# Kernel tuning notes

Measured on AMD Instinct MI355X. Metric: run time of the kernel, lower is better.

## Reference

```python
import jax, jax.numpy as jnp
import numpy as np

# --- configuration constants (from OpticalDotProductConfiguration) ---
INPUT_BITS = 8
ADC_BITS = 8
DAC_VMIN, DAC_VMAX = 0.0, 1.0
ADC_VMAX = 1.0
OPT_GAIN = 10.0
AWG_XTALK = 0.01
MZM_VMIN, MZM_VMAX = 0.0, 1.0
MZM_LOSS = 10.0 ** (-0.5 / 10.0)   # loss_dB_to_linear(0.5)
YB_LOSS = 10.0 ** (-0.3 / 10.0)
MRR_LOSS = 10.0 ** (-0.5 / 10.0)
MRR_XTALK = 0.01
PD_RESP = 1.0
PD_DARK = 1e-12
PD_R = 50.0
PD_HZ = 10.0 * 1e9
PD_T = 300.0
TIA_GAIN = 100.0
K_B = 1.380649e-23
Q_E = 1.602176634e-19

B, N = 4096, 8192


def conv_same(x, kernel):
    # x: [B, N], kernel: [K]; torch F.conv1d = cross-correlation, same as lax conv
    out = jax.lax.conv_general_dilated(
        x[:, None, :], kernel[None, None, :], (1,), 'SAME')
    return out[:, 0, :]


def setup_inputs() -> dict:
    key = jax.random.key(0)
    ks = jax.random.split(key, 6)
    return {
        'x': jax.random.normal(ks[0], (B, N), dtype=jnp.float32),
        'weights': jax.random.normal(ks[1], (N,), dtype=jnp.float32),
        'noise_tp': jax.random.normal(ks[2], (B,), dtype=jnp.float32),
        'noise_sp': jax.random.normal(ks[3], (B,), dtype=jnp.float32),
        'noise_tn': jax.random.normal(ks[4], (B,), dtype=jnp.float32),
        'noise_sn': jax.random.normal(ks[5], (B,), dtype=jnp.float32),
    }


def reference(x, weights, noise_tp, noise_sp, noise_tn, noise_sn):
    dt = x.dtype
    # software_implemented_transformation
    wnorm = jnp.max(jnp.abs(weights))
    wnorm = jnp.where(wnorm <= 1e-9, jnp.asarray(1.0, dt), wnorm)
    wt = weights / wnorm
    w_abs = jnp.abs(wt)            # weight DAC is identity for weights
    w_pos = wt >= 0                # [N] bool

    t_pos = x > 0                  # [B, N]
    ax = jnp.abs(x)
    inorm = jnp.max(ax, axis=1)
    inorm = jnp.where(inorm <= 1e-9, jnp.asarray(1.0, dt), inorm)[:, None]
    maxq_in = 2 ** INPUT_BITS - 1
    q = jnp.round(ax / inorm * maxq_in)

    # input DAC
    d = jnp.round(jnp.clip(q, 0.0, maxq_in)) / maxq_in
    d = DAC_VMIN + (DAC_VMAX - DAC_VMIN) * d

    # laser: gain + AWG crosstalk conv
    lk = jnp.array([AWG_XTALK / 4, AWG_XTALK, 1.0, AWG_XTALK, AWG_XTALK / 4], dtype=dt)
    l = conv_same(d * OPT_GAIN, lk)

    # MZM
    m = l * w_abs / (MZM_VMAX - MZM_VMIN) * (YB_LOSS * MZM_LOSS)

    # MRR: masked split, crosstalk conv, loss, reduce over N
    pm = jnp.logical_not(jnp.logical_xor(w_pos[None, :], t_pos)).astype(dt)
    mk = jnp.array([MRR_XTALK / 4, MRR_XTALK, 1.0, MRR_XTALK, MRR_XTALK / 4], dtype=dt)
    pos_sum = jnp.sum(conv_same(m * pm, mk) * MRR_LOSS, axis=1)        # [B]
    neg_sum = jnp.sum(conv_same(m * (1.0 - pm), mk) * MRR_LOSS, axis=1)

    # photodiode with injected noise
    thermal_c = 4.0 * K_B * PD_T * PD_HZ / PD_R
    shot_c = 2.0 * Q_E * PD_HZ

    def pd(t, nth, nsh):
        t = t * PD_RESP + PD_DARK
        t = t + nth * thermal_c
        return t * (1.0 + nsh * shot_c)

    cur = pd(pos_sum, noise_tp, noise_sp) - pd(neg_sum, noise_tn, noise_sn)

    # TIA
    v = jnp.abs(cur * TIA_GAIN)
    sign = (cur >= 0).astype(dt) * 2.0 - 1.0

    # ADC
    sf = (2 ** ADC_BITS - 1) / ADC_VMAX
    va = jnp.round(jnp.clip(v, 0.0, ADC_VMAX) * sf) / sf
    out = va * sign

    scale = wnorm / (2.0 ** (ADC_BITS - INPUT_BITS))
    scale = scale / (OPT_GAIN * TIA_GAIN * MRR_LOSS * YB_LOSS * MZM_LOSS)
    scale = scale / ((PD_RESP + PD_RESP) / 2.0)
    out = out * (scale * inorm[:, 0])
    return out
```

## Files before the change

### kernel.cpp

```cpp
#include <hip/hip_runtime.h>
#include <math.h>

#define NCOL 8192
#define BT   512
#define EPT  16

#define MZM_LOSS_D 0.8912509381337456
#define YB_LOSS_D  0.9332543007969910
#define MRR_LOSS_D 0.8912509381337456

__global__ __launch_bounds__(BT, 4)
void odp_main(const float* __restrict__ x, const float* __restrict__ w,
              const float* __restrict__ ntp, const float* __restrict__ nsp,
              const float* __restrict__ ntn, const float* __restrict__ nsn,
              float* __restrict__ out)
{
    __shared__ float  redf[16];
    __shared__ float  redT[8];
    __shared__ double redD[8];
    __shared__ double corrd[4];

    const int t    = threadIdx.x;
    const int lane = t & 63;
    const int wid  = t >> 6;
    const int b    = blockIdx.x;

    const float v_ntp = ntp[b], v_nsp = nsp[b], v_ntn = ntn[b], v_nsn = nsn[b];

    const float*  __restrict__ xrow = x + (size_t)b * NCOL;
    const float4* __restrict__ xr4  = (const float4*)xrow;
    const float4* __restrict__ w4   = (const float4*)w;

    float xf[EPT], wf[EPT];
    const int hL = (t > 0)      ? (t * EPT - 2)   : 0;
    const int hR = (t < BT - 1) ? (t * EPT + EPT) : (NCOL - 2);
    const float2 hxL = *(const float2*)(xrow + hL);
    const float2 hxR = *(const float2*)(xrow + hR);

    float mx = 0.f, mw = 0.f;
#pragma unroll
    for (int j = 0; j < 4; ++j) {
        const float4 xv = xr4[t * 4 + j];
        const float4 wv = w4 [t * 4 + j];
        xf[4*j+0]=xv.x; xf[4*j+1]=xv.y; xf[4*j+2]=xv.z; xf[4*j+3]=xv.w;
        wf[4*j+0]=wv.x; wf[4*j+1]=wv.y; wf[4*j+2]=wv.z; wf[4*j+3]=wv.w;
        mx = fmaxf(mx, fmaxf(fmaxf(fabsf(xv.x), fabsf(xv.y)),
                             fmaxf(fabsf(xv.z), fabsf(xv.w))));
        mw = fmaxf(mw, fmaxf(fmaxf(fabsf(wv.x), fabsf(wv.y)),
                             fmaxf(fabsf(wv.z), fabsf(wv.w))));
    }
#pragma unroll
    for (int off = 32; off; off >>= 1) {
        mx = fmaxf(mx, __shfl_down(mx, off));
        mw = fmaxf(mw, __shfl_down(mw, off));
    }
    if (lane == 0) { redf[wid] = mx; redf[8 + wid] = mw; }
    __syncthreads();

    float inorm = redf[0], wnorm = redf[8];
#pragma unroll
    for (int i = 1; i < 8; ++i) {
        inorm = fmaxf(inorm, redf[i]);
        wnorm = fmaxf(wnorm, redf[8 + i]);
    }
    inorm = (inorm <= 1e-9f) ? 1.f : inorm;
    wnorm = (wnorm <= 1e-9f) ? 1.f : wnorm;

    const double inv_d = 1.0 / (double)inorm;
    const float  y     = (float)inv_d;

    float Q[EPT + 4];
#pragma unroll
    for (int c = 0; c < EPT; ++c) {
        const float a  = fabsf(xf[c]);
        const float q0 = a * y;
        const float r  = fmaf(-inorm, q0, a);
        Q[c + 2] = rintf(fmaf(r, y, q0) * 255.f);
    }
    {
        const float aL0 = fabsf(hxL.x), aL1 = fabsf(hxL.y);
        const float aR0 = fabsf(hxR.x), aR1 = fabsf(hxR.y);
        float q0, r;
        q0 = aL0 * y; r = fmaf(-inorm, q0, aL0); Q[0]  = rintf(fmaf(r, y, q0) * 255.f);
        q0 = aL1 * y; r = fmaf(-inorm, q0, aL1); Q[1]  = rintf(fmaf(r, y, q0) * 255.f);
        q0 = aR0 * y; r = fmaf(-inorm, q0, aR0); Q[18] = rintf(fmaf(r, y, q0) * 255.f);
        q0 = aR1 * y; r = fmaf(-inorm, q0, aR1); Q[19] = rintf(fmaf(r, y, q0) * 255.f);
        if (t == 0)      { Q[0]  = 0.f; Q[1]  = 0.f; }
        if (t == BT - 1) { Q[18] = 0.f; Q[19] = 0.f; }
    }

    float Dv[4] = {0.f,0.f,0.f,0.f}, Tv[4] = {0.f,0.f,0.f,0.f};
    double cD = 0.0, cT = 0.0;
    const double DE0 = -((double)0.01f + (double)0.0025f);
    const double DE1 = -((double)0.0025f);

#pragma unroll
    for (int c = 0; c < EPT; ++c) {
        const float s1 = Q[c + 1] + Q[c + 3];
        const float s2 = Q[c]     + Q[c + 4];
        float conv = fmaf(0.01f, s1, Q[c + 2]);
        conv = fmaf(0.0025f, s2, conv);
        const float sel = (xf[c] > 0.f) ? wf[c] : -wf[c];
        Dv[c & 3] = fmaf(conv, sel,        Dv[c & 3]);
        Tv[c & 3] = fmaf(conv, fabsf(sel), Tv[c & 3]);
        if (t == 0 && c < 2) {
            const double de = (c == 0) ? DE0 : DE1;
            cD += de * (double)(conv * sel);
            cT += de * (double)(conv * fabsf(sel));
        }
        if (t == BT - 1 && c >= EPT - 2) {
            const double de = (c == EPT - 1) ? DE0 : DE1;
            cD += de * (double)(conv * sel);
            cT += de * (double)(conv * fabsf(sel));
        }
    }

    double accD = ((double)Dv[0] + (double)Dv[1]) + ((double)Dv[2] + (double)Dv[3]);
    float  accT = (Tv[0] + Tv[1]) + (Tv[2] + Tv[3]);

#pragma unroll
    for (int off = 32; off; off >>= 1) {
        accD += __shfl_down(accD, off);
        accT += __shfl_down(accT, off);
    }
    if (lane == 0)   { redD[wid] = accD; redT[wid] = accT; }
    if (t == 0)      { corrd[0] = cD; corrd[1] = cT; }
    if (t == BT - 1) { corrd[2] = cD; corrd[3] = cT; }
    __syncthreads();

    if (t == 0) {
        double D = 0.0, T = 0.0;
#pragma unroll
        for (int i = 0; i < 8; ++i) { D += redD[i]; T += (double)redT[i]; }
        const double E_MID = 1.0 + 2.0 * (double)0.01f + 2.0 * (double)0.0025f;
        D = D * E_MID + (corrd[0] + corrd[2]);
        T = T * E_MID + (corrd[1] + corrd[3]);

        const double Kd = (10.0 / 255.0) * (YB_LOSS_D * MZM_LOSS_D) / (double)wnorm;
        const double ps = (T + D) * 0.5 * Kd * MRR_LOSS_D;
        const double ns = (T - D) * 0.5 * Kd * MRR_LOSS_D;

        const float thermal_f = 3.3135576e-12f;
        const float shot_f    = 3.204353268e-9f;

        double tp_ = ps + 1e-12 + (double)(v_ntp * thermal_f);
        tp_ *= (double)(1.0f + v_nsp * shot_f);
        double tn_ = ns + 1e-12 + (double)(v_ntn * thermal_f);
        tn_ *= (double)(1.0f + v_nsn * shot_f);

        const double cur = tp_ - tn_;
        double v = fabs(cur * 100.0);
        v = fmin(v, 1.0);
        const double va  = rint(v * 255.0) * (1.0 / 255.0);
        const double sgn = (cur >= 0.0) ? 1.0 : -1.0;
        const double scale = (double)wnorm /
            (10.0 * 100.0 * MRR_LOSS_D * YB_LOSS_D * MZM_LOSS_D);
        out[b] = (float)(va * sgn * scale * (double)inorm);
    }
}

extern "C" void kernel_launch(void* const* d_in, const int* in_sizes, int n_in,
                              void* d_out, int out_size, void* d_ws, size_t ws_size,
                              hipStream_t stream) {
    const float* x   = (const float*)d_in[0];
    const float* w   = (const float*)d_in[1];
    const float* ntp = (const float*)d_in[2];
    const float* nsp = (const float*)d_in[3];
    const float* ntn = (const float*)d_in[4];
    const float* nsn = (const float*)d_in[5];
    float* out = (float*)d_out;
    odp_main<<<dim3(out_size), dim3(BT), 0, stream>>>(x, w, ntp, nsp, ntn, nsn, out);
}
```

Baseline: 30.31 us.

## Halve block size, double elements per thread, defer weight-norm reduction

```diff
diff --git a/kernel.cpp b/kernel.cpp
--- a/kernel.cpp
+++ b/kernel.cpp
@@ -2,12 +2,24 @@
 #include <math.h>
 
 #define NCOL 8192
-#define BT   512
-#define EPT  16
+#define BT   256
+#define EPT  32
 
 #define MZM_LOSS_D 0.8912509381337456
 #define YB_LOSS_D  0.9332543007969910
 #define MRR_LOSS_D 0.8912509381337456
+
+static __device__ __forceinline__ void lds_barrier() {
+    asm volatile("s_waitcnt lgkmcnt(0)" ::: "memory");
+    __builtin_amdgcn_s_barrier();
+}
+
+#define QF(dst, a_) do {                                   \
+    const float a__  = (a_);                               \
+    const float q0__ = a__ * y;                            \
+    const float r__  = fmaf(-inorm, q0__, a__);            \
+    (dst) = rintf(fmaf(r__, y, q0__) * 255.f);             \
+} while (0)
 
 __global__ __launch_bounds__(BT, 4)
 void odp_main(const float* __restrict__ x, const float* __restrict__ w,
@@ -15,9 +27,10 @@
               const float* __restrict__ ntn, const float* __restrict__ nsn,
               float* __restrict__ out)
 {
-    __shared__ float  redf[16];
-    __shared__ float  redT[8];
-    __shared__ double redD[8];
+    __shared__ float  redX[4];
+    __shared__ float  redW[4];
+    __shared__ float  redT[4];
+    __shared__ double redD[4];
     __shared__ double corrd[4];
 
     const int t    = threadIdx.x;
@@ -32,88 +45,81 @@
     const float4* __restrict__ w4   = (const float4*)w;
 
     float xf[EPT], wf[EPT];
-    const int hL = (t > 0)      ? (t * EPT - 2)   : 0;
-    const int hR = (t < BT - 1) ? (t * EPT + EPT) : (NCOL - 2);
-    const float2 hxL = *(const float2*)(xrow + hL);
-    const float2 hxR = *(const float2*)(xrow + hR);
-
     float mx = 0.f, mw = 0.f;
 #pragma unroll
-    for (int j = 0; j < 4; ++j) {
-        const float4 xv = xr4[t * 4 + j];
-        const float4 wv = w4 [t * 4 + j];
+    for (int j = 0; j < 8; ++j) {
+        const float4 xv = xr4[t * 8 + j];
         xf[4*j+0]=xv.x; xf[4*j+1]=xv.y; xf[4*j+2]=xv.z; xf[4*j+3]=xv.w;
-        wf[4*j+0]=wv.x; wf[4*j+1]=wv.y; wf[4*j+2]=wv.z; wf[4*j+3]=wv.w;
         mx = fmaxf(mx, fmaxf(fmaxf(fabsf(xv.x), fabsf(xv.y)),
                              fmaxf(fabsf(xv.z), fabsf(xv.w))));
+    }
+    const float2 hxL = *(const float2*)(xrow + ((t > 0)      ? t*EPT - 2   : 0));
+    const float2 hxR = *(const float2*)(xrow + ((t < BT - 1) ? t*EPT + EPT : NCOL - 2));
+#pragma unroll
+    for (int j = 0; j < 8; ++j) {
+        const float4 wv = w4[t * 8 + j];
+        wf[4*j+0]=wv.x; wf[4*j+1]=wv.y; wf[4*j+2]=wv.z; wf[4*j+3]=wv.w;
         mw = fmaxf(mw, fmaxf(fmaxf(fabsf(wv.x), fabsf(wv.y)),
                              fmaxf(fabsf(wv.z), fabsf(wv.w))));
     }
+
 #pragma unroll
-    for (int off = 32; off; off >>= 1) {
+    for (int off = 32; off; off >>= 1)
         mx = fmaxf(mx, __shfl_down(mx, off));
-        mw = fmaxf(mw, __shfl_down(mw, off));
-    }
-    if (lane == 0) { redf[wid] = mx; redf[8 + wid] = mw; }
-    __syncthreads();
+    if (lane == 0) redX[wid] = mx;
+    lds_barrier();
 
-    float inorm = redf[0], wnorm = redf[8];
-#pragma unroll
-    for (int i = 1; i < 8; ++i) {
-        inorm = fmaxf(inorm, redf[i]);
-        wnorm = fmaxf(wnorm, redf[8 + i]);
-    }
+    float inorm = fmaxf(fmaxf(redX[0], redX[1]), fmaxf(redX[2], redX[3]));
     inorm = (inorm <= 1e-9f) ? 1.f : inorm;
-    wnorm = (wnorm <= 1e-9f) ? 1.f : wnorm;
-
     const double inv_d = 1.0 / (double)inorm;
     const float  y     = (float)inv_d;
-
-    float Q[EPT + 4];
-#pragma unroll
-    for (int c = 0; c < EPT; ++c) {
-        const float a  = fabsf(xf[c]);
-        const float q0 = a * y;
-        const float r  = fmaf(-inorm, q0, a);
-        Q[c + 2] = rintf(fmaf(r, y, q0) * 255.f);
-    }
-    {
-        const float aL0 = fabsf(hxL.x), aL1 = fabsf(hxL.y);
-        const float aR0 = fabsf(hxR.x), aR1 = fabsf(hxR.y);
-        float q0, r;
-        q0 = aL0 * y; r = fmaf(-inorm, q0, aL0); Q[0]  = rintf(fmaf(r, y, q0) * 255.f);
-        q0 = aL1 * y; r = fmaf(-inorm, q0, aL1); Q[1]  = rintf(fmaf(r, y, q0) * 255.f);
-        q0 = aR0 * y; r = fmaf(-inorm, q0, aR0); Q[18] = rintf(fmaf(r, y, q0) * 255.f);
-        q0 = aR1 * y; r = fmaf(-inorm, q0, aR1); Q[19] = rintf(fmaf(r, y, q0) * 255.f);
-        if (t == 0)      { Q[0]  = 0.f; Q[1]  = 0.f; }
-        if (t == BT - 1) { Q[18] = 0.f; Q[19] = 0.f; }
-    }
 
     float Dv[4] = {0.f,0.f,0.f,0.f}, Tv[4] = {0.f,0.f,0.f,0.f};
     double cD = 0.0, cT = 0.0;
     const double DE0 = -((double)0.01f + (double)0.0025f);
     const double DE1 = -((double)0.0025f);
 
-#pragma unroll
-    for (int c = 0; c < EPT; ++c) {
-        const float s1 = Q[c + 1] + Q[c + 3];
-        const float s2 = Q[c]     + Q[c + 4];
-        float conv = fmaf(0.01f, s1, Q[c + 2]);
-        conv = fmaf(0.0025f, s2, conv);
-        const float sel = (xf[c] > 0.f) ? wf[c] : -wf[c];
-        Dv[c & 3] = fmaf(conv, sel,        Dv[c & 3]);
-        Tv[c & 3] = fmaf(conv, fabsf(sel), Tv[c & 3]);
-        if (t == 0 && c < 2) {
-            const double de = (c == 0) ? DE0 : DE1;
-            cD += de * (double)(conv * sel);
-            cT += de * (double)(conv * fabsf(sel));
-        }
-        if (t == BT - 1 && c >= EPT - 2) {
-            const double de = (c == EPT - 1) ? DE0 : DE1;
-            cD += de * (double)(conv * sel);
-            cT += de * (double)(conv * fabsf(sel));
-        }
-    }
+#define HALF_BODY(H) do {                                                     \
+    float Q[20];                                                              \
+    if ((H) == 0) {                                                           \
+        QF(Q[0], fabsf(hxL.x)); QF(Q[1], fabsf(hxL.y));                       \
+        if (t == 0) { Q[0] = 0.f; Q[1] = 0.f; }                               \
+    } else {                                                                  \
+        QF(Q[0], fabsf(xf[14])); QF(Q[1], fabsf(xf[15]));                     \
+    }                                                                         \
+    _Pragma("unroll")                                                         \
+    for (int cc = 0; cc < 16; ++cc) QF(Q[cc + 2], fabsf(xf[(H)*16 + cc]));    \
+    if ((H) == 0) {                                                           \
+        QF(Q[18], fabsf(xf[16])); QF(Q[19], fabsf(xf[17]));                   \
+    } else {                                                                  \
+        QF(Q[18], fabsf(hxR.x)); QF(Q[19], fabsf(hxR.y));                     \
+        if (t == BT - 1) { Q[18] = 0.f; Q[19] = 0.f; }                        \
+    }                                                                         \
+    _Pragma("unroll")                                                         \
+    for (int cc = 0; cc < 16; ++cc) {                                         \
+        const int idx = (H)*16 + cc;                                          \
+        const float s1 = Q[cc + 1] + Q[cc + 3];                               \
+        const float s2 = Q[cc]     + Q[cc + 4];                               \
+        float cv = fmaf(0.01f, s1, Q[cc + 2]);                                \
+        cv = fmaf(0.0025f, s2, cv);                                           \
+        const float sel = (xf[idx] > 0.f) ? wf[idx] : -wf[idx];               \
+        Dv[cc & 3] = fmaf(cv, sel,        Dv[cc & 3]);                        \
+        Tv[cc & 3] = fmaf(cv, fabsf(sel), Tv[cc & 3]);                        \
+        if ((H) == 0 && t == 0 && cc < 2) {                                   \
+            const double de = (cc == 0) ? DE0 : DE1;                          \
+            cD += de * (double)(cv * sel);                                    \
+            cT += de * (double)(cv * fabsf(sel));                             \
+        }                                                                     \
+        if ((H) == 1 && t == BT - 1 && cc >= 14) {                            \
+            const double de = (cc == 15) ? DE0 : DE1;                         \
+            cD += de * (double)(cv * sel);                                    \
+            cT += de * (double)(cv * fabsf(sel));                             \
+        }                                                                     \
+    }                                                                         \
+} while (0)
+
+    HALF_BODY(0);
+    HALF_BODY(1);
 
     double accD = ((double)Dv[0] + (double)Dv[1]) + ((double)Dv[2] + (double)Dv[3]);
     float  accT = (Tv[0] + Tv[1]) + (Tv[2] + Tv[3]);
@@ -122,16 +128,23 @@
     for (int off = 32; off; off >>= 1) {
         accD += __shfl_down(accD, off);
         accT += __shfl_down(accT, off);
+        mw    = fmaxf(mw, __shfl_down(mw, off));
     }
-    if (lane == 0)   { redD[wid] = accD; redT[wid] = accT; }
+    if (lane == 0)   { redD[wid] = accD; redT[wid] = accT; redW[wid] = mw; }
     if (t == 0)      { corrd[0] = cD; corrd[1] = cT; }
     if (t == BT - 1) { corrd[2] = cD; corrd[3] = cT; }
-    __syncthreads();
+    lds_barrier();
 
     if (t == 0) {
         double D = 0.0, T = 0.0;
+        float wnorm = redW[0];
 #pragma unroll
-        for (int i = 0; i < 8; ++i) { D += redD[i]; T += (double)redT[i]; }
+        for (int i = 0; i < 4; ++i) {
+            D += redD[i]; T += (double)redT[i];
+            wnorm = fmaxf(wnorm, redW[i]);
+        }
+        wnorm = (wnorm <= 1e-9f) ? 1.f : wnorm;
+
         const double E_MID = 1.0 + 2.0 * (double)0.01f + 2.0 * (double)0.0025f;
         D = D * E_MID + (corrd[0] + corrd[2]);
         T = T * E_MID + (corrd[1] + corrd[3]);
```

Result: slower. 43.19 us (+42.5%).
